# Kernel optimization log

Measured on AMD Instinct MI355X. Metric: run time of the kernel, lower is better.

Reference implementation:

```python
import jax, jax.numpy as jnp
import numpy as np

EPS = 1e-8


def _entropy_1d(p):
    # entropy() helper with input_as_probabilities=True on a 1-D tensor:
    # clamp to EPS, x*log(x), return -sum
    p_ = jnp.maximum(p, EPS)
    return -jnp.sum(p_ * jnp.log(p_))


def setup_inputs() -> dict:
    key = jax.random.key(0)
    k1, k2 = jax.random.split(key)
    b, n = 65536, 512
    anchors = jax.random.normal(k1, (b, n), dtype=jnp.float32)
    neighbors = jax.random.normal(k2, (b, n), dtype=jnp.float32)
    return {"anchors": anchors, "neighbors": neighbors}


def reference(anchors, neighbors):
    entropy_weight = 2.0
    b, n = anchors.shape

    anchors_prob = jax.nn.softmax(anchors, axis=1)      # [b, n]
    positives_prob = jax.nn.softmax(neighbors, axis=1)  # [b, n]

    # bmm of [b,1,n] x [b,n,1] -> row-wise dot product, shape [b]
    similarity = jnp.einsum('bn,bn->b', anchors_prob, positives_prob)

    # BCELoss(similarity, ones) = -mean(log(sim)); torch clamps log at -100
    consistency_loss = -jnp.mean(jnp.maximum(jnp.log(similarity), -100.0))

    lg_sim = jnp.log(similarity)

    entropy_loss = _entropy_1d(jnp.mean(anchors_prob, axis=0))

    # cross/second-order: dot of clamped sim with clamped log-sim
    second_order_loss = jnp.dot(jnp.maximum(similarity, EPS),
                                jnp.maximum(lg_sim, EPS))

    # np.tile(sim, n).reshape(n, b) then view(b, n, 1): equivalent to the
    # flat [b*n] tiled vector reshaped row-major to [b, n]
    tiled_sim = jnp.tile(similarity, n).reshape(b, n)
    third_order_entropy = jnp.einsum('bn,bn->b', anchors_prob, tiled_sim)
    lg_third = jnp.log(third_order_entropy)
    third_order_loss = jnp.dot(jnp.maximum(third_order_entropy, EPS),
                               jnp.maximum(lg_third, EPS)) / n

    third_weight = 0.5 / np.sqrt(n)
    diff_weight = 0.25 / n

    total_loss = (consistency_loss
                  - entropy_weight * entropy_loss
                  + diff_weight * second_order_loss
                  - third_weight * third_order_loss)
    return (total_loss, consistency_loss, entropy_loss,
            second_order_loss, third_order_loss)
```

## Files before the change

kernel.cpp:

```cpp
#include <hip/hip_runtime.h>
#include <math.h>

#define B_ROWS 65536
#define N_COLS 512
#define EPS 1e-8f
#define GRID1 2048


__global__ __launch_bounds__(256, 8) void k_main(
        const float* __restrict__ A, const float* __restrict__ Bn,
        float* __restrict__ sim, float* __restrict__ colsum,
        float* __restrict__ acc) {
    __shared__ float cs[512];
    __shared__ float sred[16];
    const int t    = threadIdx.x;
    const int lane = t & 63;
    const int w    = t >> 6;
    const int s    = blockIdx.x & 127;
    const int kb   = (blockIdx.x >> 7) * 32 + w * 8;

    cs[t] = 0.f; cs[t + 256] = 0.f;

    float cacc[8];
#pragma unroll
    for (int k = 0; k < 8; ++k) cacc[k] = 0.f;
    float accLog = 0.f, accSim = 0.f;

    size_t off = (size_t)(s + 128 * kb) * N_COLS + lane * 4;

#pragma unroll 1
    for (int r = 0; r < 8; ++r) {
        const float4 a0 = *(const float4*)(A  + off);
        const float4 a1 = *(const float4*)(A  + off + 256);
        const float4 b0 = *(const float4*)(Bn + off);
        const float4 b1 = *(const float4*)(Bn + off + 256);

        const float av[8] = {a0.x, a0.y, a0.z, a0.w, a1.x, a1.y, a1.z, a1.w};
        const float bv[8] = {b0.x, b0.y, b0.z, b0.w, b1.x, b1.y, b1.z, b1.w};
        float ea[8];
        float sA = 0.f, sB = 0.f, d = 0.f;
#pragma unroll
        for (int k = 0; k < 8; ++k) {
            float e = __expf(av[k]);
            float f = __expf(bv[k]);
            ea[k] = e;
            sA += e; sB += f; d += e * f;
        }
#pragma unroll
        for (int m = 32; m >= 1; m >>= 1) {
            sA += __shfl_xor(sA, m, 64);
            sB += __shfl_xor(sB, m, 64);
            d  += __shfl_xor(d,  m, 64);
        }
        float inv_sa = 1.f / sA;
#pragma unroll
        for (int k = 0; k < 8; ++k) cacc[k] += ea[k] * inv_sa;
        if (lane == 0) {
            float sv = d * inv_sa * (1.f / sB);
            sim[s + 128 * (kb + r)] = sv;
            accLog += fmaxf(__logf(sv), -100.f);
            accSim += fmaxf(sv, EPS);
        }
        off += (size_t)128 * N_COLS;
    }

    if (lane == 0) { sred[w] = accLog; sred[8 + w] = accSim; }
    __syncthreads();
#pragma unroll
    for (int k = 0; k < 4; ++k) atomicAdd(&cs[lane * 4 + k], cacc[k]);
#pragma unroll
    for (int k = 0; k < 4; ++k) atomicAdd(&cs[256 + lane * 4 + k], cacc[4 + k]);
    __syncthreads();

    float* cdst = colsum + (size_t)s * 512;
    atomicAdd(&cdst[t], cs[t]);
    atomicAdd(&cdst[t + 256], cs[t + 256]);
    if (t == 0) atomicAdd(&acc[0], sred[0] + sred[1] + sred[2] + sred[3]);
    if (t == 1) atomicAdd(&acc[1], sred[8] + sred[9] + sred[10] + sred[11]);
}

__global__ __launch_bounds__(512) void k_red(
        const float* __restrict__ colsum, const float* __restrict__ sim,
        float* __restrict__ colTot, float* __restrict__ acc) {
    __shared__ float red[8];
    const int t = threadIdx.x, lane = t & 63, w = t >> 6;
    const int s0 = blockIdx.x * 2;
    float tot = 0.f, toe = 0.f;
#pragma unroll
    for (int k = 0; k < 2; ++k) {
        int idx = (s0 + k) * 512 + t;
        float c = colsum[idx];
        tot += c;
        toe += c * sim[idx];
    }
    atomicAdd(&colTot[t], tot);
#pragma unroll
    for (int m = 32; m >= 1; m >>= 1) toe += __shfl_xor(toe, m, 64);
    if (lane == 0) red[w] = toe;
    __syncthreads();
    if (t == 0) {
        float tt = red[0] + red[1] + red[2] + red[3]
                 + red[4] + red[5] + red[6] + red[7];
        atomicAdd(&acc[2], tt);
    }
}

__global__ __launch_bounds__(512) void k_fin(
        const float* __restrict__ colTot, const float* __restrict__ acc,
        float* __restrict__ out) {
    __shared__ float red[8];
    const int t = threadIdx.x, lane = t & 63, w = t >> 6;
    float p   = fmaxf(colTot[t] * (1.f / B_ROWS), EPS);
    float ent = -p * __logf(p);
#pragma unroll
    for (int m = 32; m >= 1; m >>= 1) ent += __shfl_xor(ent, m, 64);
    if (lane == 0) red[w] = ent;
    __syncthreads();
    if (t == 0) {
        float entropy = red[0] + red[1] + red[2] + red[3]
                      + red[4] + red[5] + red[6] + red[7];
        float consistency = -acc[0] * (1.f / B_ROWS);
        float second      = acc[1] * EPS;
        float third       = acc[2] * EPS * (1.f / N_COLS);
        float third_weight = 0.5f / sqrtf((float)N_COLS);
        float diff_weight  = 0.25f / (float)N_COLS;
        out[0] = consistency - 2.0f * entropy + diff_weight * second
                 - third_weight * third;
        out[1] = consistency;
        out[2] = entropy;
        out[3] = second;
        out[4] = third;
    }
}

extern "C" void kernel_launch(void* const* d_in, const int* in_sizes, int n_in,
                              void* d_out, int out_size, void* d_ws, size_t ws_size,
                              hipStream_t stream) {
    const float* anchors   = (const float*)d_in[0];
    const float* neighbors = (const float*)d_in[1];
    float* out = (float*)d_out;

    float* sim    = (float*)d_ws;
    float* colsum = sim + B_ROWS;
    float* colTot = colsum + 128 * 512;
    float* acc    = colTot + 512;

    hipMemsetAsync(colsum, 0, (128 * 512 + 512 + 16) * sizeof(float), stream);

    k_main<<<dim3(GRID1), dim3(256), 0, stream>>>(
        anchors, neighbors, sim, colsum, acc);
    k_red<<<dim3(64), dim3(512), 0, stream>>>(colsum, sim, colTot, acc);
    k_fin<<<dim3(1), dim3(512), 0, stream>>>(colTot, acc, out);
}
```

Before: 298.9 us.

## Restructure main kernel to process contiguous row groups with LDS slab accumulation

The main kernel now uses 512-thread blocks, 512 in total, each covering contiguous groups of 8 rows per 128-row stripe instead of strided rows. Each wave issues loads for 4 rows at once to raise memory-level parallelism, and accumulates column probabilities into an 8x512 shared-memory slab with LDS atomics. Each block then flushes the slab to the global colsum buckets. The aim is more coalesced DRAM access and more loads in flight, at the cost of many LDS atomics per row and more global atomics at flush time.

Result: slower. 387.1 us (+29.5%).

```diff
diff --git a/kernel.cpp b/kernel.cpp
--- a/kernel.cpp
+++ b/kernel.cpp
@@ -4,79 +4,102 @@
 #define B_ROWS 65536
 #define N_COLS 512
 #define EPS 1e-8f
-#define GRID1 2048
 
 
-__global__ __launch_bounds__(256, 8) void k_main(
+__global__ __launch_bounds__(512, 4) void k_main(
         const float* __restrict__ A, const float* __restrict__ Bn,
         float* __restrict__ sim, float* __restrict__ colsum,
         float* __restrict__ acc) {
-    __shared__ float cs[512];
+    __shared__ float slab[8 * 512];
     __shared__ float sred[16];
     const int t    = threadIdx.x;
     const int lane = t & 63;
     const int w    = t >> 6;
-    const int s    = blockIdx.x & 127;
-    const int kb   = (blockIdx.x >> 7) * 32 + w * 8;
+    const int g    = blockIdx.x & 15;
+    const int q    = blockIdx.x >> 4;
 
-    cs[t] = 0.f; cs[t + 256] = 0.f;
+    for (int i = t; i < 8 * 512; i += 512) slab[i] = 0.f;
+    __syncthreads();
 
-    float cacc[8];
-#pragma unroll
-    for (int k = 0; k < 8; ++k) cacc[k] = 0.f;
     float accLog = 0.f, accSim = 0.f;
 
-    size_t off = (size_t)(s + 128 * kb) * N_COLS + lane * 4;
+#pragma unroll 1
+    for (int kk = 0; kk < 2; ++kk) {
+        const int k = q * 16 + w * 2 + kk;
+        const int rowIdx0 = 128 * k + 8 * g;
+        const size_t rowbase = (size_t)rowIdx0 * N_COLS;
 
 #pragma unroll 1
-    for (int r = 0; r < 8; ++r) {
-        const float4 a0 = *(const float4*)(A  + off);
-        const float4 a1 = *(const float4*)(A  + off + 256);
-        const float4 b0 = *(const float4*)(Bn + off);
-        const float4 b1 = *(const float4*)(Bn + off + 256);
-
-        const float av[8] = {a0.x, a0.y, a0.z, a0.w, a1.x, a1.y, a1.z, a1.w};
-        const float bv[8] = {b0.x, b0.y, b0.z, b0.w, b1.x, b1.y, b1.z, b1.w};
-        float ea[8];
-        float sA = 0.f, sB = 0.f, d = 0.f;
+        for (int jb = 0; jb < 8; jb += 4) {
+            int dd[4];
+            float4 A0[4], A1[4], B0[4], B1[4];
 #pragma unroll
-        for (int k = 0; k < 8; ++k) {
-            float e = __expf(av[k]);
-            float f = __expf(bv[k]);
-            ea[k] = e;
-            sA += e; sB += f; d += e * f;
+            for (int i = 0; i < 4; ++i) {
+                const int d = ((jb + i) + w) & 7;
+                dd[i] = d;
+                const float* ap = A  + rowbase + d * N_COLS + lane * 4;
+                const float* bp = Bn + rowbase + d * N_COLS + lane * 4;
+                A0[i] = *(const float4*)ap;
+                A1[i] = *(const float4*)(ap + 256);
+                B0[i] = *(const float4*)bp;
+                B1[i] = *(const float4*)(bp + 256);
+            }
+#pragma unroll
+            for (int i = 0; i < 4; ++i) {
+                const float av[8] = {A0[i].x, A0[i].y, A0[i].z, A0[i].w,
+                                     A1[i].x, A1[i].y, A1[i].z, A1[i].w};
+                const float bv[8] = {B0[i].x, B0[i].y, B0[i].z, B0[i].w,
+                                     B1[i].x, B1[i].y, B1[i].z, B1[i].w};
+                float ea[8];
+                float sA = 0.f, sB = 0.f, dp = 0.f;
+#pragma unroll
+                for (int c = 0; c < 8; ++c) {
+                    float e = __expf(av[c]);
+                    float f = __expf(bv[c]);
+                    ea[c] = e;
+                    sA += e; sB += f; dp += e * f;
+                }
+#pragma unroll
+                for (int m = 32; m >= 1; m >>= 1) {
+                    sA += __shfl_xor(sA, m, 64);
+                    sB += __shfl_xor(sB, m, 64);
+                    dp += __shfl_xor(dp, m, 64);
+                }
+                const float inv = 1.f / sA;
+                float* sl = slab + dd[i] * 512;
+#pragma unroll
+                for (int c = 0; c < 4; ++c)
+                    atomicAdd(&sl[c * 128 + lane], ea[c] * inv);
+#pragma unroll
+                for (int c = 0; c < 4; ++c)
+                    atomicAdd(&sl[c * 128 + 64 + lane], ea[4 + c] * inv);
+                if (lane == 0) {
+                    float sv = dp * inv * (1.f / sB);
+                    sim[rowIdx0 + dd[i]] = sv;
+                    accLog += fmaxf(__logf(sv), -100.f);
+                    accSim += fmaxf(sv, EPS);
+                }
+            }
         }
-#pragma unroll
-        for (int m = 32; m >= 1; m >>= 1) {
-            sA += __shfl_xor(sA, m, 64);
-            sB += __shfl_xor(sB, m, 64);
-            d  += __shfl_xor(d,  m, 64);
-        }
-        float inv_sa = 1.f / sA;
-#pragma unroll
-        for (int k = 0; k < 8; ++k) cacc[k] += ea[k] * inv_sa;
-        if (lane == 0) {
-            float sv = d * inv_sa * (1.f / sB);
-            sim[s + 128 * (kb + r)] = sv;
-            accLog += fmaxf(__logf(sv), -100.f);
-            accSim += fmaxf(sv, EPS);
-        }
-        off += (size_t)128 * N_COLS;
     }
 
     if (lane == 0) { sred[w] = accLog; sred[8 + w] = accSim; }
     __syncthreads();
+
+    {
+        const int c = t >> 7, m = t & 127;
+        const int j = (m < 64) ? (m * 4 + c) : (256 + (m - 64) * 4 + c);
 #pragma unroll
-    for (int k = 0; k < 4; ++k) atomicAdd(&cs[lane * 4 + k], cacc[k]);
+        for (int d = 0; d < 8; ++d)
+            atomicAdd(&colsum[(size_t)(8 * g + d) * 512 + j], slab[d * 512 + t]);
+    }
+    if (t == 0) {
+        float l = 0.f, s2 = 0.f;
 #pragma unroll
-    for (int k = 0; k < 4; ++k) atomicAdd(&cs[256 + lane * 4 + k], cacc[4 + k]);
-    __syncthreads();
-
-    float* cdst = colsum + (size_t)s * 512;
-    atomicAdd(&cdst[t], cs[t]);
-    atomicAdd(&cdst[t + 256], cs[t + 256]);
-    if (t == 0) atomicAdd(&acc[0], sred[0] + sred[1] + sred[2] + sred[3]);
-    if (t == 1) atomicAdd(&acc[1], sred[8] + sred[9] + sred[10] + sred[11]);
+        for (int i = 0; i < 8; ++i) { l += sred[i]; s2 += sred[8 + i]; }
+        atomicAdd(&acc[0], l);
+        atomicAdd(&acc[1], s2);
+    }
 }
 
 __global__ __launch_bounds__(512) void k_red(
@@ -147,7 +170,7 @@
 
     hipMemsetAsync(colsum, 0, (128 * 512 + 512 + 16) * sizeof(float), stream);
 
-    k_main<<<dim3(GRID1), dim3(256), 0, stream>>>(
+    k_main<<<dim3(512), dim3(512), 0, stream>>>(
         anchors, neighbors, sim, colsum, acc);
     k_red<<<dim3(64), dim3(512), 0, stream>>>(colsum, sim, colTot, acc);
     k_fin<<<dim3(1), dim3(512), 0, stream>>>(colTot, acc, out);
```

## Prefetch rows into LDS with async global_load_lds triple-buffer pipeline

Applied to the files above, without the earlier changes.

Replaces the per-row direct float4 global loads with asynchronous global-to-LDS loads staged three rows ahead in a four-slot per-wave ring buffer, then reads each row back from LDS after a vmcnt wait. The aim is to keep more memory requests in flight per wave in this bandwidth-bound softmax/dot kernel. It adds 64 KB of LDS per block and drops the occupancy hint from launch_bounds, which limits how many blocks can be resident per CU. It also relies on manual vmcnt counting that must match the interleaved sim stores.

Measured after the change: 299.1 us. No clear change (+0.1%).

```diff
diff --git a/kernel.cpp b/kernel.cpp
--- a/kernel.cpp
+++ b/kernel.cpp
@@ -7,10 +7,18 @@
 #define GRID1 2048
 
 
-__global__ __launch_bounds__(256, 8) void k_main(
+typedef const __attribute__((address_space(1))) void glb_v;
+typedef __attribute__((address_space(3))) void lds_v;
+
+#define GLLDS(g, l) \
+    __builtin_amdgcn_global_load_lds((glb_v*)(g), (lds_v*)(l), 16, 0, 0)
+#define WAITVM(n) asm volatile("s_waitcnt vmcnt(" #n ")" ::: "memory")
+
+__global__ __launch_bounds__(256) void k_main(
         const float* __restrict__ A, const float* __restrict__ Bn,
         float* __restrict__ sim, float* __restrict__ colsum,
         float* __restrict__ acc) {
+    __shared__ float tile[4][4][1024];
     __shared__ float cs[512];
     __shared__ float sred[16];
     const int t    = threadIdx.x;
@@ -26,43 +34,66 @@
     for (int k = 0; k < 8; ++k) cacc[k] = 0.f;
     float accLog = 0.f, accSim = 0.f;
 
-    size_t off = (size_t)(s + 128 * kb) * N_COLS + lane * 4;
+    const size_t rowbase = (size_t)(s + 128 * kb) * N_COLS;
+    const float* Ab = A  + rowbase + lane * 4;
+    const float* Bb = Bn + rowbase + lane * 4;
+    const size_t rstride = (size_t)128 * N_COLS;
+    float* myt = &tile[w][0][0];
 
-#pragma unroll 1
-    for (int r = 0; r < 8; ++r) {
-        const float4 a0 = *(const float4*)(A  + off);
-        const float4 a1 = *(const float4*)(A  + off + 256);
-        const float4 b0 = *(const float4*)(Bn + off);
-        const float4 b1 = *(const float4*)(Bn + off + 256);
+#define STAGE(r) do {                                                   \
+        float* sl_ = myt + ((r) & 3) * 1024;                            \
+        const float* ga_ = Ab + (size_t)(r) * rstride;                  \
+        const float* gb_ = Bb + (size_t)(r) * rstride;                  \
+        GLLDS(ga_,       sl_);                                          \
+        GLLDS(ga_ + 256, sl_ + 256);                                    \
+        GLLDS(gb_,       sl_ + 512);                                    \
+        GLLDS(gb_ + 256, sl_ + 768);                                    \
+    } while (0)
 
-        const float av[8] = {a0.x, a0.y, a0.z, a0.w, a1.x, a1.y, a1.z, a1.w};
-        const float bv[8] = {b0.x, b0.y, b0.z, b0.w, b1.x, b1.y, b1.z, b1.w};
-        float ea[8];
-        float sA = 0.f, sB = 0.f, d = 0.f;
-#pragma unroll
-        for (int k = 0; k < 8; ++k) {
-            float e = __expf(av[k]);
-            float f = __expf(bv[k]);
-            ea[k] = e;
-            sA += e; sB += f; d += e * f;
-        }
-#pragma unroll
-        for (int m = 32; m >= 1; m >>= 1) {
-            sA += __shfl_xor(sA, m, 64);
-            sB += __shfl_xor(sB, m, 64);
-            d  += __shfl_xor(d,  m, 64);
-        }
-        float inv_sa = 1.f / sA;
-#pragma unroll
-        for (int k = 0; k < 8; ++k) cacc[k] += ea[k] * inv_sa;
-        if (lane == 0) {
-            float sv = d * inv_sa * (1.f / sB);
-            sim[s + 128 * (kb + r)] = sv;
-            accLog += fmaxf(__logf(sv), -100.f);
-            accSim += fmaxf(sv, EPS);
-        }
-        off += (size_t)128 * N_COLS;
-    }
+    STAGE(0); STAGE(1); STAGE(2);
+
+#define ROWSTEP(r, VM) do {                                             \
+        if ((r) + 3 < 8) STAGE((r) + 3);                                \
+        WAITVM(VM);  \
+        const float* sl_ = myt + ((r) & 3) * 1024;                      \
+        const float4 a0 = *(const float4*)(sl_ + lane * 4);             \
+        const float4 a1 = *(const float4*)(sl_ + 256 + lane * 4);       \
+        const float4 b0 = *(const float4*)(sl_ + 512 + lane * 4);      \
+        const float4 b1 = *(const float4*)(sl_ + 768 + lane * 4);      \
+        const float av[8] = {a0.x, a0.y, a0.z, a0.w,                    \
+                             a1.x, a1.y, a1.z, a1.w};                   \
+        const float bv[8] = {b0.x, b0.y, b0.z, b0.w,                    \
+                             b1.x, b1.y, b1.z, b1.w};                   \
+        float ea[8];                                                    \
+        float sA = 0.f, sB = 0.f, dp = 0.f;                             \
+        _Pragma("unroll")                                               \
+        for (int c = 0; c < 8; ++c) {                                   \
+            float e = __expf(av[c]);                                    \
+            float f = __expf(bv[c]);                                    \
+            ea[c] = e;                                                  \
+            sA += e; sB += f; dp += e * f;                              \
+        }                                                               \
+        _Pragma("unroll")                                               \
+        for (int m = 32; m >= 1; m >>= 1) {                             \
+            sA += __shfl_xor(sA, m, 64);                                \
+            sB += __shfl_xor(sB, m, 64);                                \
+            dp += __shfl_xor(dp, m, 64);                                \
+        }                                                               \
+        const float inv = 1.f / sA;                                     \
+        _Pragma("unroll")                                               \
+        for (int c = 0; c < 8; ++c) cacc[c] += ea[c] * inv;             \
+        if (lane == 0) {                                                \
+            float sv = dp * inv * (1.f / sB);                           \
+            sim[s + 128 * (kb + (r))] = sv;                             \
+            accLog += fmaxf(__logf(sv), -100.f);                        \
+            accSim += fmaxf(sv, EPS);                                   \
+        }                                                               \
+    } while (0)
+
+    ROWSTEP(0, 12); ROWSTEP(1, 12); ROWSTEP(2, 12); ROWSTEP(3, 12);
+    ROWSTEP(4, 12); ROWSTEP(5, 8);  ROWSTEP(6, 4);  ROWSTEP(7, 0);
+#undef ROWSTEP
+#undef STAGE
 
     if (lane == 0) { sred[w] = accLog; sred[8 + w] = accSim; }
     __syncthreads();
```

## Batch four row loads per wave and remap rows to grid-strided global indices

Applied to the files above, without the earlier changes.

Each wave now issues loads for four rows at once, two batches of four, instead of walking eight rows one at a time. This raises memory-level parallelism and interleaves the shuffle reductions across the four rows. Row assignment changes to a grid-strided global index, which still keeps rows with the same index mod 128 in the same colsum slot. The per-wave column sums now go to separate shared-memory slices and no longer use shared atomics. Each block then issues four global atomic rows instead of one, and register pressure rises now that the occupancy hint is gone.

Result: faster. 290.5 us (-2.8%).

```diff
diff --git a/kernel.cpp b/kernel.cpp
--- a/kernel.cpp
+++ b/kernel.cpp
@@ -7,74 +7,91 @@
 #define GRID1 2048
 
 
-__global__ __launch_bounds__(256, 8) void k_main(
+__global__ __launch_bounds__(256) void k_main(
         const float* __restrict__ A, const float* __restrict__ Bn,
         float* __restrict__ sim, float* __restrict__ colsum,
         float* __restrict__ acc) {
-    __shared__ float cs[512];
+    __shared__ float cs[4][512];
     __shared__ float sred[16];
     const int t    = threadIdx.x;
     const int lane = t & 63;
     const int w    = t >> 6;
-    const int s    = blockIdx.x & 127;
-    const int kb   = (blockIdx.x >> 7) * 32 + w * 8;
-
-    cs[t] = 0.f; cs[t + 256] = 0.f;
+    const int g    = blockIdx.x * 4 + w;
 
     float cacc[8];
 #pragma unroll
     for (int k = 0; k < 8; ++k) cacc[k] = 0.f;
     float accLog = 0.f, accSim = 0.f;
 
-    size_t off = (size_t)(s + 128 * kb) * N_COLS + lane * 4;
-
-#pragma unroll 1
-    for (int r = 0; r < 8; ++r) {
-        const float4 a0 = *(const float4*)(A  + off);
-        const float4 a1 = *(const float4*)(A  + off + 256);
-        const float4 b0 = *(const float4*)(Bn + off);
-        const float4 b1 = *(const float4*)(Bn + off + 256);
-
-        const float av[8] = {a0.x, a0.y, a0.z, a0.w, a1.x, a1.y, a1.z, a1.w};
-        const float bv[8] = {b0.x, b0.y, b0.z, b0.w, b1.x, b1.y, b1.z, b1.w};
-        float ea[8];
-        float sA = 0.f, sB = 0.f, d = 0.f;
 #pragma unroll
-        for (int k = 0; k < 8; ++k) {
-            float e = __expf(av[k]);
-            float f = __expf(bv[k]);
-            ea[k] = e;
-            sA += e; sB += f; d += e * f;
+    for (int batch = 0; batch < 2; ++batch) {
+        int rows[4];
+        float4 a0[4], a1[4], b0[4], b1[4];
+#pragma unroll
+        for (int q = 0; q < 4; ++q) {
+            rows[q] = g + 8192 * (batch * 4 + q);
+            const float* a = A  + (size_t)rows[q] * N_COLS;
+            const float* b = Bn + (size_t)rows[q] * N_COLS;
+            a0[q] = *(const float4*)(a + lane * 4);
+            a1[q] = *(const float4*)(a + 256 + lane * 4);
+            b0[q] = *(const float4*)(b + lane * 4);
+            b1[q] = *(const float4*)(b + 256 + lane * 4);
+        }
+        float ea[4][8], sa[4], sb[4], dp[4];
+#pragma unroll
+        for (int q = 0; q < 4; ++q) {
+            float av[8] = {a0[q].x, a0[q].y, a0[q].z, a0[q].w,
+                           a1[q].x, a1[q].y, a1[q].z, a1[q].w};
+            float bv[8] = {b0[q].x, b0[q].y, b0[q].z, b0[q].w,
+                           b1[q].x, b1[q].y, b1[q].z, b1[q].w};
+            float sA = 0.f, sB = 0.f, d = 0.f;
+#pragma unroll
+            for (int k = 0; k < 8; ++k) {
+                float e = __expf(av[k]);
+                float f = __expf(bv[k]);
+                ea[q][k] = e;
+                sA += e; sB += f; d += e * f;
+            }
+            sa[q] = sA; sb[q] = sB; dp[q] = d;
         }
 #pragma unroll
         for (int m = 32; m >= 1; m >>= 1) {
-            sA += __shfl_xor(sA, m, 64);
-            sB += __shfl_xor(sB, m, 64);
-            d  += __shfl_xor(d,  m, 64);
+#pragma unroll
+            for (int q = 0; q < 4; ++q) {
+                sa[q] += __shfl_xor(sa[q], m, 64);
+                sb[q] += __shfl_xor(sb[q], m, 64);
+                dp[q] += __shfl_xor(dp[q], m, 64);
+            }
         }
-        float inv_sa = 1.f / sA;
 #pragma unroll
-        for (int k = 0; k < 8; ++k) cacc[k] += ea[k] * inv_sa;
-        if (lane == 0) {
-            float sv = d * inv_sa * (1.f / sB);
-            sim[s + 128 * (kb + r)] = sv;
-            accLog += fmaxf(__logf(sv), -100.f);
-            accSim += fmaxf(sv, EPS);
+        for (int q = 0; q < 4; ++q) {
+            float inv_sa = 1.f / sa[q];
+#pragma unroll
+            for (int k = 0; k < 8; ++k) cacc[k] += ea[q][k] * inv_sa;
+            if (lane == 0) {
+                float sv = dp[q] * inv_sa * (1.f / sb[q]);
+                sim[rows[q]] = sv;
+                float lg = __logf(sv);
+                accLog += fmaxf(lg, -100.f);
+                accSim += fmaxf(sv, EPS);
+            }
         }
-        off += (size_t)128 * N_COLS;
     }
 
     if (lane == 0) { sred[w] = accLog; sred[8 + w] = accSim; }
-    __syncthreads();
 #pragma unroll
-    for (int k = 0; k < 4; ++k) atomicAdd(&cs[lane * 4 + k], cacc[k]);
+    for (int k = 0; k < 4; ++k) cs[w][lane * 4 + k] = cacc[k];
 #pragma unroll
-    for (int k = 0; k < 4; ++k) atomicAdd(&cs[256 + lane * 4 + k], cacc[4 + k]);
+    for (int k = 0; k < 4; ++k) cs[w][256 + lane * 4 + k] = cacc[4 + k];
     __syncthreads();
 
-    float* cdst = colsum + (size_t)s * 512;
-    atomicAdd(&cdst[t], cs[t]);
-    atomicAdd(&cdst[t + 256], cs[t + 256]);
+#pragma unroll
+    for (int ww = 0; ww < 4; ++ww) {
+        const int sw = (blockIdx.x * 4 + ww) & 127;
+        float* cdst = colsum + (size_t)sw * 512;
+        atomicAdd(&cdst[t], cs[ww][t]);
+        atomicAdd(&cdst[t + 256], cs[ww][t + 256]);
+    }
     if (t == 0) atomicAdd(&acc[0], sred[0] + sred[1] + sred[2] + sred[3]);
     if (t == 1) atomicAdd(&acc[1], sred[8] + sred[9] + sred[10] + sred[11]);
 }
```
